# Optimization experiments

Measured on AMD Instinct MI355X. Metric: run time of the kernel, lower is better.

Reference implementation:

```python
import jax, jax.numpy as jnp
import numpy as np

BS, Z, NOBJ = 16384, 512, 64


def setup_inputs() -> dict:
    key = jax.random.key(0)
    ks = jax.random.split(key, 12)
    din = Z + 4  # z concatenated with bounds (x_size = 0)

    def lin(k, i, o):
        kw, kb = jax.random.split(k)
        w = jax.random.normal(kw, (i, o), jnp.float32) * (1.0 / np.sqrt(i))
        b = jax.random.normal(kb, (o,), jnp.float32) * 0.01
        return w, b

    W1, c1 = lin(ks[0], din, 512)
    W2, c2 = lin(ks[1], 512, 256)
    W3, c3 = lin(ks[2], 256, 128)
    W4, c4 = lin(ks[3], 128, 64)
    W5, c5 = lin(ks[4], 64, NOBJ * 4)
    z = jax.random.normal(ks[5], (BS, Z), jnp.float32)
    # room bounds [x_min, y_min, x_max, y_max]; must allow gaps >= 1
    bounds = jnp.array([0.0, 0.0, 40.0, 40.0], jnp.float32)
    return {"z": z, "bounds": bounds,
            "W1": W1, "c1": c1, "W2": W2, "c2": c2, "W3": W3, "c3": c3,
            "W4": W4, "c4": c4, "W5": W5, "c5": c5}


def _lrelu(v):
    return jnp.where(v > 0, v, 0.2 * v)


def _solve_axis(pp, pg, lo, hi):
    """Exact KKT solution of: min (x-pp)^2 + (g-pg)^2  s.t. x>=lo, g>=1, x+g<=hi.
    Returns (x, w) with w = x + g. Matches the parabolic QP per object/axis."""
    x0 = jnp.maximum(pp, lo)          # box projection (lower bounds only)
    g0 = jnp.maximum(pg, 1.0)
    t = 0.5 * (hi - pp - pg)          # projection of (pp,pg) onto line x+g=hi
    xl = jnp.clip(pp + t, lo, hi - 1.0)
    over = (x0 + g0) > hi             # coupling constraint active?
    x = jnp.where(over, xl, x0)
    g = jnp.where(over, hi - xl, g0)
    return x, x + g


def reference(z, bounds, W1, c1, W2, c2, W3, c3, W4, c4, W5, c5):
    bs = z.shape[0]
    bnd = jnp.broadcast_to(bounds, (bs, 4))
    h = jnp.concatenate([z, bnd], axis=1)          # (bs, z_size+4)
    h = _lrelu(h @ W1 + c1)                        # dropout treated as eval/identity
    h = _lrelu(h @ W2 + c2)
    h = _lrelu(h @ W3 + c3)
    h = _lrelu(h @ W4 + c4)
    p = (h @ W5 + c5).reshape(bs, NOBJ, 4)         # per-object params [px, py, pw, ph]
    px, py, pw, ph = p[..., 0], p[..., 1], p[..., 2], p[..., 3]
    b0, b1, b2, b3 = bounds[0], bounds[1], bounds[2], bounds[3]
    # QP objective: sum (x-px)^2+(y-py)^2+((w-x)-pw)^2+((h-y)-ph)^2
    # s.t. x>=b0, y>=b1, w<=b2, h<=b3, x<=w-1, y<=h-1. Separable per object/axis.
    xs, ws = _solve_axis(px, pw, b0, b2)
    ys, hs = _solve_axis(py, ph, b1, b3)
    return jnp.stack([xs, ys, ws, hs], axis=-1)    # (bs, num_objs, 4)
```

## Files before the change

kernel.cpp:

```cpp
#include <hip/hip_runtime.h>


#define MROWS 16384

typedef __attribute__((ext_vector_type(8))) short bf16x8;
typedef __attribute__((ext_vector_type(4))) float floatx4;

__device__ __forceinline__ unsigned short f2bf(float x) {
    union { float f; unsigned u; } c; c.f = x;
    unsigned r = c.u + 0x7fffu + ((c.u >> 16) & 1u);
    return (unsigned short)(r >> 16);
}
__device__ __forceinline__ float bf2f(unsigned short b) {
    union { unsigned u; float f; } c; c.u = ((unsigned)b) << 16;
    return c.f;
}

__device__ __forceinline__ bf16x8 gload(const unsigned short* p) {
    bf16x8 r;
    asm volatile("global_load_dwordx4 %0, %1, off"
                 : "=&v"(r)
                 : "v"((unsigned long long)(size_t)p)
                 : "memory");
    return r;
}
template<int IMM>
__device__ __forceinline__ void vwait(bf16x8& v) {
    asm volatile("s_waitcnt vmcnt(%1)" : "+v"(v) : "n"(IMM) : "memory");
}
__device__ __forceinline__ void drain8(bf16x8 (&r)[8]) {
    asm volatile("s_waitcnt vmcnt(0)"
                 : "+v"(r[0]), "+v"(r[1]), "+v"(r[2]), "+v"(r[3]),
                   "+v"(r[4]), "+v"(r[5]), "+v"(r[6]), "+v"(r[7])
                 :: "memory");
}
__device__ __forceinline__ void drain4(bf16x8 (&r)[4]) {
    asm volatile("s_waitcnt vmcnt(0)"
                 : "+v"(r[0]), "+v"(r[1]), "+v"(r[2]), "+v"(r[3])
                 :: "memory");
}

__global__ __launch_bounds__(256) void pack_wt(
    const float* __restrict__ W1, unsigned short* __restrict__ T1,
    const float* __restrict__ W2, unsigned short* __restrict__ T2,
    const float* __restrict__ W3, unsigned short* __restrict__ T3,
    const float* __restrict__ W4, unsigned short* __restrict__ T4,
    const float* __restrict__ W5, unsigned short* __restrict__ T5)
{
    const int idx = blockIdx.x * 256 + threadIdx.x;
    if (blockIdx.y == 4) {
        if (idx >= 256 * 64) return;
        const int k = idx >> 8, n = idx & 255;
        const float v = W5[idx];
        const unsigned short hi = f2bf(v);
        const unsigned short lo = f2bf(v - bf2f(hi));
        const int ntile = n >> 4, m_l = n & 15;
        const int ks = k >> 5, quad = (k >> 3) & 3, e = k & 7;
        const size_t b = (size_t)(((ks * 16 + ntile) * 2) * 64 + quad * 16 + m_l) * 8 + e;
        T5[b] = hi; T5[b + 512] = lo;
        return;
    }
    const float* W; unsigned short* T; int Kreal, nshift;
    switch (blockIdx.y) {
        case 0:  W = W1; T = T1; Kreal = 516; nshift = 9; break;
        case 1:  W = W2; T = T2; Kreal = 512; nshift = 8; break;
        case 2:  W = W3; T = T3; Kreal = 256; nshift = 7; break;
        default: W = W4; T = T4; Kreal = 128; nshift = 6; break;
    }
    const int N = 1 << nshift, NT = N >> 4;
    const int KS = (Kreal + 31) >> 5;
    if (idx >= N * KS * 32) return;
    const int k = idx >> nshift;
    const int n = idx & (N - 1);
    const unsigned short v = (k < Kreal) ? f2bf(W[idx]) : (unsigned short)0;
    const int ntile = n >> 4, m_l = n & 15;
    const int ks = k >> 5, quad = (k >> 3) & 3, e = k & 7;
    T[(size_t)((ks * NT + ntile) * 64 + quad * 16 + m_l) * 8 + e] = v;
}

#define OFF_ZS   0
#define LD_ZS    552
#define OFF_H1   17664
#define LD_H1    520
#define OFF_H2   0
#define LD_H2    264
#define OFF_H3   17664
#define LD_H3    136
#define OFF_H4   8448
#define LD_H4    72
#define OFF_P    17664
#define LD_P     260
#define LDS_TOT  34304

template<int NF, int KSTEPS, int NT, int DEP>
__device__ __forceinline__ void layer_stream(
    unsigned short* lds, int offA, int lda, int offC, int ldc,
    const unsigned short* __restrict__ Wt,
    const float* __restrict__ bias, int wid, int lane)
{
    const int m_l = lane & 15, quad = lane >> 4;
    constexpr int NFR = NF * KSTEPS;
    const unsigned short* __restrict__ Wb = Wt + ((size_t)(wid * NF) * 64 + lane) * 8;

    floatx4 acc[2][NF];
    #pragma unroll
    for (int j = 0; j < NF; ++j) {
        const float bv = bias[wid * (NF * 16) + j * 16 + m_l];
        acc[0][j] = (floatx4){bv, bv, bv, bv};
        acc[1][j] = (floatx4){bv, bv, bv, bv};
    }

    bf16x8 ring[DEP];
    #pragma unroll
    for (int f = 0; f < DEP; ++f) {
        const int g = (f < NFR) ? f : 0;
        ring[f] = gload(Wb + (size_t)((g / NF) * NT + (g % NF)) * 512);
    }
    bf16x8 a0, a1;
    #pragma unroll
    for (int f = 0; f < NFR; ++f) {
        const int ks = f / NF, j = f - ks * NF;
        if (j == 0) {
            a0 = *(const bf16x8*)&lds[offA + (m_l     ) * lda + ks*32 + quad*8];
            a1 = *(const bf16x8*)&lds[offA + (m_l + 16) * lda + ks*32 + quad*8];
        }
        vwait<DEP - 1>(ring[f % DEP]);
        acc[0][j] = __builtin_amdgcn_mfma_f32_16x16x32_bf16(a0, ring[f % DEP], acc[0][j], 0, 0, 0);
        acc[1][j] = __builtin_amdgcn_mfma_f32_16x16x32_bf16(a1, ring[f % DEP], acc[1][j], 0, 0, 0);
        const int nf2 = (f + DEP < NFR) ? f + DEP : 0;
        ring[f % DEP] = gload(Wb + (size_t)((nf2 / NF) * NT + (nf2 % NF)) * 512);
    }
    if constexpr (DEP == 8) drain8(ring); else drain4(ring);

    #pragma unroll
    for (int j = 0; j < NF; ++j) {
        const int col = wid * (NF * 16) + j * 16 + m_l;
        #pragma unroll
        for (int i = 0; i < 2; ++i)
            #pragma unroll
            for (int r = 0; r < 4; ++r) {
                float v = acc[i][j][r];
                v = v > 0.f ? v : 0.2f * v;
                lds[offC + (i*16 + quad*4 + r) * ldc + col] = f2bf(v);
            }
    }
}

__global__ __launch_bounds__(256, 2) void fused_mlp_qp(
    const float* __restrict__ z, const float* __restrict__ bounds,
    const unsigned short* __restrict__ Wt1, const float* __restrict__ c1,
    const unsigned short* __restrict__ Wt2, const float* __restrict__ c2,
    const unsigned short* __restrict__ Wt3, const float* __restrict__ c3,
    const unsigned short* __restrict__ Wt4, const float* __restrict__ c4,
    const unsigned short* __restrict__ Wt5, const float* __restrict__ c5,
    float* __restrict__ out)
{
    __shared__ unsigned short lds[LDS_TOT];
    const int tid  = threadIdx.x;
    const int wid  = tid >> 6, lane = tid & 63;
    const int m_l  = lane & 15, quad = lane >> 4;
    const int bm   = blockIdx.x * 32;

    const float4 bnd = *(const float4*)bounds;

    {
        const float4* __restrict__ zf = (const float4*)(z + (size_t)bm * 512);
        #pragma unroll
        for (int i = 0; i < 16; ++i) {
            const int f   = i * 256 + tid;
            const int row = f >> 7, c4i = f & 127;
            const float4 v = zf[f];
            unsigned short t4[4] = {f2bf(v.x), f2bf(v.y), f2bf(v.z), f2bf(v.w)};
            *(uint2*)&lds[OFF_ZS + row * LD_ZS + c4i * 4] = *(uint2*)t4;
        }
        if (tid < 160) {
            const int row = tid / 5, j = tid % 5;
            unsigned short t8[8] = {0,0,0,0,0,0,0,0};
            if (j == 0) { t8[0] = f2bf(bnd.x); t8[1] = f2bf(bnd.y);
                          t8[2] = f2bf(bnd.z); t8[3] = f2bf(bnd.w); }
            *(uint4*)&lds[OFF_ZS + row * LD_ZS + 512 + j * 8] = *(uint4*)t8;
        }
    }
    __syncthreads();

    layer_stream<8,17,32,8>(lds, OFF_ZS, LD_ZS, OFF_H1, LD_H1, Wt1, c1, wid, lane);
    __syncthreads();
    layer_stream<4,16,16,8>(lds, OFF_H1, LD_H1, OFF_H2, LD_H2, Wt2, c2, wid, lane);
    __syncthreads();
    layer_stream<2,8, 8, 8>(lds, OFF_H2, LD_H2, OFF_H3, LD_H3, Wt3, c3, wid, lane);
    __syncthreads();
    layer_stream<1,4, 4, 4>(lds, OFF_H3, LD_H3, OFF_H4, LD_H4, Wt4, c4, wid, lane);
    __syncthreads();

    {
        const unsigned short* __restrict__ Wb5 = Wt5 + (size_t)wid * 4096 + (size_t)lane * 8;
        floatx4 acc[2][4];
        #pragma unroll
        for (int j = 0; j < 4; ++j) {
            const float bv = c5[wid * 64 + j * 16 + m_l];
            acc[0][j] = (floatx4){bv, bv, bv, bv};
            acc[1][j] = (floatx4){bv, bv, bv, bv};
        }
        auto w5off = [](int g) {
            const int ks = g >> 3, rem = g & 7;
            return (size_t)ks * 16384 + (size_t)(rem >> 1) * 1024 + (size_t)(rem & 1) * 512;
        };
        bf16x8 ring[8];
        #pragma unroll
        for (int f = 0; f < 8; ++f) ring[f] = gload(Wb5 + w5off(f));
        bf16x8 a0, a1;
        #pragma unroll
        for (int f = 0; f < 16; ++f) {
            const int ks = f >> 3, rem = f & 7, j = rem >> 1;
            if (rem == 0) {
                a0 = *(const bf16x8*)&lds[OFF_H4 + (m_l     ) * LD_H4 + ks*32 + quad*8];
                a1 = *(const bf16x8*)&lds[OFF_H4 + (m_l + 16) * LD_H4 + ks*32 + quad*8];
            }
            vwait<7>(ring[f & 7]);
            acc[0][j] = __builtin_amdgcn_mfma_f32_16x16x32_bf16(a0, ring[f & 7], acc[0][j], 0, 0, 0);
            acc[1][j] = __builtin_amdgcn_mfma_f32_16x16x32_bf16(a1, ring[f & 7], acc[1][j], 0, 0, 0);
            const int nf2 = (f + 8 < 16) ? f + 8 : 0;
            ring[f & 7] = gload(Wb5 + w5off(nf2));
        }
        drain8(ring);

        float* __restrict__ p = (float*)&lds[OFF_P];
        #pragma unroll
        for (int j = 0; j < 4; ++j) {
            const int col = wid * 64 + j * 16 + m_l;
            #pragma unroll
            for (int i = 0; i < 2; ++i)
                #pragma unroll
                for (int r = 0; r < 4; ++r)
                    p[(i*16 + quad*4 + r) * LD_P + col] = acc[i][j][r];
        }
    }
    __syncthreads();

    const float b0 = bnd.x, b1 = bnd.y, b2 = bnd.z, b3 = bnd.w;
    const float* __restrict__ p = (const float*)&lds[OFF_P];
    #pragma unroll
    for (int i = 0; i < 8; ++i) {
        const int row = i * 4 + wid;
        const float4 pv = *(const float4*)&p[row * LD_P + lane * 4];
        float xs, wo, ys, ho;
        {
            const float px = pv.x, pw = pv.z;
            const float x0 = fmaxf(px, b0);
            const float g0 = fmaxf(pw, 1.0f);
            const float t  = 0.5f * (b2 - px - pw);
            const float xl = fminf(fmaxf(px + t, b0), b2 - 1.0f);
            const bool over = (x0 + g0) > b2;
            const float x = over ? xl : x0;
            const float g = over ? (b2 - xl) : g0;
            xs = x; wo = x + g;
        }
        {
            const float py = pv.y, ph = pv.w;
            const float x0 = fmaxf(py, b1);
            const float g0 = fmaxf(ph, 1.0f);
            const float t  = 0.5f * (b3 - py - ph);
            const float xl = fminf(fmaxf(py + t, b1), b3 - 1.0f);
            const bool over = (x0 + g0) > b3;
            const float x = over ? xl : x0;
            const float g = over ? (b3 - xl) : g0;
            ys = x; ho = x + g;
        }
        float4 o; o.x = xs; o.y = ys; o.z = wo; o.w = ho;
        ((float4*)out)[(size_t)(bm + row) * 64 + lane] = o;
    }
}

extern "C" void kernel_launch(void* const* d_in, const int* in_sizes, int n_in,
                              void* d_out, int out_size, void* d_ws, size_t ws_size,
                              hipStream_t stream) {
    const float* z      = (const float*)d_in[0];
    const float* bounds = (const float*)d_in[1];
    const float* W1 = (const float*)d_in[2];
    const float* c1 = (const float*)d_in[3];
    const float* W2 = (const float*)d_in[4];
    const float* c2 = (const float*)d_in[5];
    const float* W3 = (const float*)d_in[6];
    const float* c3 = (const float*)d_in[7];
    const float* W4 = (const float*)d_in[8];
    const float* c4 = (const float*)d_in[9];
    const float* W5 = (const float*)d_in[10];
    const float* c5 = (const float*)d_in[11];
    float* out = (float*)d_out;

    unsigned short* ws  = (unsigned short*)d_ws;
    unsigned short* Wt1 = ws;
    unsigned short* Wt2 = Wt1 + 278528;
    unsigned short* Wt3 = Wt2 + 131072;
    unsigned short* Wt4 = Wt3 + 32768;
    unsigned short* Wt5 = Wt4 + 8192;

    pack_wt<<<dim3(1088, 5), 256, 0, stream>>>(
        W1, Wt1, W2, Wt2, W3, Wt3, W4, Wt4, W5, Wt5);
    fused_mlp_qp<<<dim3(MROWS / 32), 256, 0, stream>>>(
        z, bounds, Wt1, c1, Wt2, c2, Wt3, c3, Wt4, c4, Wt5, c5, out);
}
```

Baseline: 124.7 us.

## Double row tile to 64 per block with 8 waves and vectorize weight packing

The fused MLP block now handles 64 rows with 512 threads (8 waves). Each wave computes 4 M-fragments per streamed weight fragment, which halves per-row weight traffic from L2 and reuses each B fragment across more MFMAs. LDS usage doubles to about 134 KB, which may limit occupancy to one block per CU. The weight-pack kernel now has each thread build 8 K-elements and write them with one 16-byte store, replacing per-element scattered stores.

Result: faster. 120.5 us (-3.4%).

```diff
diff --git a/kernel.cpp b/kernel.cpp
--- a/kernel.cpp
+++ b/kernel.cpp
@@ -49,15 +49,20 @@
 {
     const int idx = blockIdx.x * 256 + threadIdx.x;
     if (blockIdx.y == 4) {
-        if (idx >= 256 * 64) return;
-        const int k = idx >> 8, n = idx & 255;
-        const float v = W5[idx];
-        const unsigned short hi = f2bf(v);
-        const unsigned short lo = f2bf(v - bf2f(hi));
+        if (idx >= 2048) return;
+        const int k8 = idx >> 8, n = idx & 255;
+        const int ks = k8 >> 2, quad = k8 & 3;
         const int ntile = n >> 4, m_l = n & 15;
-        const int ks = k >> 5, quad = (k >> 3) & 3, e = k & 7;
-        const size_t b = (size_t)(((ks * 16 + ntile) * 2) * 64 + quad * 16 + m_l) * 8 + e;
-        T5[b] = hi; T5[b + 512] = lo;
+        unsigned short hi8[8], lo8[8];
+        #pragma unroll
+        for (int e = 0; e < 8; ++e) {
+            const float v = W5[(k8 * 8 + e) * 256 + n];
+            const unsigned short hi = f2bf(v);
+            hi8[e] = hi; lo8[e] = f2bf(v - bf2f(hi));
+        }
+        const size_t b = (size_t)(((ks * 16 + ntile) * 2) * 64 + quad * 16 + m_l) * 8;
+        *(uint4*)&T5[b]       = *(const uint4*)hi8;
+        *(uint4*)&T5[b + 512] = *(const uint4*)lo8;
         return;
     }
     const float* W; unsigned short* T; int Kreal, nshift;
@@ -69,45 +74,50 @@
     }
     const int N = 1 << nshift, NT = N >> 4;
     const int KS = (Kreal + 31) >> 5;
-    if (idx >= N * KS * 32) return;
-    const int k = idx >> nshift;
-    const int n = idx & (N - 1);
-    const unsigned short v = (k < Kreal) ? f2bf(W[idx]) : (unsigned short)0;
+    if (idx >= N * KS * 4) return;
+    const int k8 = idx >> nshift, n = idx & (N - 1);
+    const int ks = k8 >> 2, quad = k8 & 3;
     const int ntile = n >> 4, m_l = n & 15;
-    const int ks = k >> 5, quad = (k >> 3) & 3, e = k & 7;
-    T[(size_t)((ks * NT + ntile) * 64 + quad * 16 + m_l) * 8 + e] = v;
+    unsigned short t8[8];
+    #pragma unroll
+    for (int e = 0; e < 8; ++e) {
+        const int k = k8 * 8 + e;
+        t8[e] = (k < Kreal) ? f2bf(W[(size_t)k * N + n]) : (unsigned short)0;
+    }
+    *(uint4*)&T[(size_t)((ks * NT + ntile) * 64 + quad * 16 + m_l) * 8] = *(const uint4*)t8;
 }
 
 #define OFF_ZS   0
 #define LD_ZS    552
-#define OFF_H1   17664
+#define OFF_H1   35328
 #define LD_H1    520
 #define OFF_H2   0
 #define LD_H2    264
-#define OFF_H3   17664
+#define OFF_H3   16896
 #define LD_H3    136
-#define OFF_H4   8448
+#define OFF_H4   25600
 #define LD_H4    72
-#define OFF_P    17664
+#define OFF_P    35328
 #define LD_P     260
-#define LDS_TOT  34304
-
-template<int NF, int KSTEPS, int NT, int DEP>
+#define LDS_TOT  68608
+
+template<int MR, int NF, int KSTEPS, int NT, int DEP>
 __device__ __forceinline__ void layer_stream(
     unsigned short* lds, int offA, int lda, int offC, int ldc,
     const unsigned short* __restrict__ Wt,
-    const float* __restrict__ bias, int wid, int lane)
+    const float* __restrict__ bias, int ntile0, int rowbase, int lane)
 {
     const int m_l = lane & 15, quad = lane >> 4;
     constexpr int NFR = NF * KSTEPS;
-    const unsigned short* __restrict__ Wb = Wt + ((size_t)(wid * NF) * 64 + lane) * 8;
-
-    floatx4 acc[2][NF];
+    const unsigned short* __restrict__ Wb = Wt + ((size_t)ntile0 * 64 + lane) * 8;
+
+    floatx4 acc[MR][NF];
     #pragma unroll
     for (int j = 0; j < NF; ++j) {
-        const float bv = bias[wid * (NF * 16) + j * 16 + m_l];
-        acc[0][j] = (floatx4){bv, bv, bv, bv};
-        acc[1][j] = (floatx4){bv, bv, bv, bv};
+        const float bv = bias[ntile0 * 16 + j * 16 + m_l];
+        #pragma unroll
+        for (int m = 0; m < MR; ++m)
+            acc[m][j] = (floatx4){bv, bv, bv, bv};
     }
 
     bf16x8 ring[DEP];
@@ -116,17 +126,19 @@
         const int g = (f < NFR) ? f : 0;
         ring[f] = gload(Wb + (size_t)((g / NF) * NT + (g % NF)) * 512);
     }
-    bf16x8 a0, a1;
+    bf16x8 a[MR];
     #pragma unroll
     for (int f = 0; f < NFR; ++f) {
         const int ks = f / NF, j = f - ks * NF;
         if (j == 0) {
-            a0 = *(const bf16x8*)&lds[offA + (m_l     ) * lda + ks*32 + quad*8];
-            a1 = *(const bf16x8*)&lds[offA + (m_l + 16) * lda + ks*32 + quad*8];
+            #pragma unroll
+            for (int m = 0; m < MR; ++m)
+                a[m] = *(const bf16x8*)&lds[offA + (rowbase + m*16 + m_l) * lda + ks*32 + quad*8];
         }
         vwait<DEP - 1>(ring[f % DEP]);
-        acc[0][j] = __builtin_amdgcn_mfma_f32_16x16x32_bf16(a0, ring[f % DEP], acc[0][j], 0, 0, 0);
-        acc[1][j] = __builtin_amdgcn_mfma_f32_16x16x32_bf16(a1, ring[f % DEP], acc[1][j], 0, 0, 0);
+        #pragma unroll
+        for (int m = 0; m < MR; ++m)
+            acc[m][j] = __builtin_amdgcn_mfma_f32_16x16x32_bf16(a[m], ring[f % DEP], acc[m][j], 0, 0, 0);
         const int nf2 = (f + DEP < NFR) ? f + DEP : 0;
         ring[f % DEP] = gload(Wb + (size_t)((nf2 / NF) * NT + (nf2 % NF)) * 512);
     }
@@ -134,19 +146,19 @@
 
     #pragma unroll
     for (int j = 0; j < NF; ++j) {
-        const int col = wid * (NF * 16) + j * 16 + m_l;
-        #pragma unroll
-        for (int i = 0; i < 2; ++i)
+        const int col = ntile0 * 16 + j * 16 + m_l;
+        #pragma unroll
+        for (int m = 0; m < MR; ++m)
             #pragma unroll
             for (int r = 0; r < 4; ++r) {
-                float v = acc[i][j][r];
+                float v = acc[m][j][r];
                 v = v > 0.f ? v : 0.2f * v;
-                lds[offC + (i*16 + quad*4 + r) * ldc + col] = f2bf(v);
+                lds[offC + (rowbase + m*16 + quad*4 + r) * ldc + col] = f2bf(v);
             }
     }
 }
 
-__global__ __launch_bounds__(256, 2) void fused_mlp_qp(
+__global__ __launch_bounds__(512, 2) void fused_mlp_qp(
     const float* __restrict__ z, const float* __restrict__ bounds,
     const unsigned short* __restrict__ Wt1, const float* __restrict__ c1,
     const unsigned short* __restrict__ Wt2, const float* __restrict__ c2,
@@ -159,7 +171,7 @@
     const int tid  = threadIdx.x;
     const int wid  = tid >> 6, lane = tid & 63;
     const int m_l  = lane & 15, quad = lane >> 4;
-    const int bm   = blockIdx.x * 32;
+    const int bm   = blockIdx.x * 64;
 
     const float4 bnd = *(const float4*)bounds;
 
@@ -167,13 +179,13 @@
         const float4* __restrict__ zf = (const float4*)(z + (size_t)bm * 512);
         #pragma unroll
         for (int i = 0; i < 16; ++i) {
-            const int f   = i * 256 + tid;
+            const int f   = i * 512 + tid;
             const int row = f >> 7, c4i = f & 127;
             const float4 v = zf[f];
             unsigned short t4[4] = {f2bf(v.x), f2bf(v.y), f2bf(v.z), f2bf(v.w)};
             *(uint2*)&lds[OFF_ZS + row * LD_ZS + c4i * 4] = *(uint2*)t4;
         }
-        if (tid < 160) {
+        if (tid < 320) {
             const int row = tid / 5, j = tid % 5;
             unsigned short t8[8] = {0,0,0,0,0,0,0,0};
             if (j == 0) { t8[0] = f2bf(bnd.x); t8[1] = f2bf(bnd.y);
@@ -183,56 +195,59 @@
     }
     __syncthreads();
 
-    layer_stream<8,17,32,8>(lds, OFF_ZS, LD_ZS, OFF_H1, LD_H1, Wt1, c1, wid, lane);
-    __syncthreads();
-    layer_stream<4,16,16,8>(lds, OFF_H1, LD_H1, OFF_H2, LD_H2, Wt2, c2, wid, lane);
-    __syncthreads();
-    layer_stream<2,8, 8, 8>(lds, OFF_H2, LD_H2, OFF_H3, LD_H3, Wt3, c3, wid, lane);
-    __syncthreads();
-    layer_stream<1,4, 4, 4>(lds, OFF_H3, LD_H3, OFF_H4, LD_H4, Wt4, c4, wid, lane);
+    layer_stream<4,2,17,32,8>(lds, OFF_ZS, LD_ZS, OFF_H1, LD_H1, Wt1, c1, wid*4,     0, lane);
+    layer_stream<4,2,17,32,8>(lds, OFF_ZS, LD_ZS, OFF_H1, LD_H1, Wt1, c1, wid*4 + 2, 0, lane);
+    __syncthreads();
+    layer_stream<4,2,16,16,8>(lds, OFF_H1, LD_H1, OFF_H2, LD_H2, Wt2, c2, wid*2, 0, lane);
+    __syncthreads();
+    layer_stream<4,1, 8, 8,8>(lds, OFF_H2, LD_H2, OFF_H3, LD_H3, Wt3, c3, wid, 0, lane);
+    __syncthreads();
+    layer_stream<2,1, 4, 4,4>(lds, OFF_H3, LD_H3, OFF_H4, LD_H4, Wt4, c4, wid & 3, (wid >> 2) * 32, lane);
     __syncthreads();
 
     {
-        const unsigned short* __restrict__ Wb5 = Wt5 + (size_t)wid * 4096 + (size_t)lane * 8;
-        floatx4 acc[2][4];
-        #pragma unroll
-        for (int j = 0; j < 4; ++j) {
-            const float bv = c5[wid * 64 + j * 16 + m_l];
-            acc[0][j] = (floatx4){bv, bv, bv, bv};
-            acc[1][j] = (floatx4){bv, bv, bv, bv};
+        const unsigned short* __restrict__ Wb5 = Wt5 + (size_t)wid * 2048 + (size_t)lane * 8;
+        floatx4 acc[4][2];
+        #pragma unroll
+        for (int j = 0; j < 2; ++j) {
+            const float bv = c5[wid * 32 + j * 16 + m_l];
+            #pragma unroll
+            for (int m = 0; m < 4; ++m)
+                acc[m][j] = (floatx4){bv, bv, bv, bv};
         }
         auto w5off = [](int g) {
-            const int ks = g >> 3, rem = g & 7;
+            const int ks = g >> 2, rem = g & 3;
             return (size_t)ks * 16384 + (size_t)(rem >> 1) * 1024 + (size_t)(rem & 1) * 512;
         };
         bf16x8 ring[8];
         #pragma unroll
         for (int f = 0; f < 8; ++f) ring[f] = gload(Wb5 + w5off(f));
-        bf16x8 a0, a1;
-        #pragma unroll
-        for (int f = 0; f < 16; ++f) {
-            const int ks = f >> 3, rem = f & 7, j = rem >> 1;
+        bf16x8 a[4];
+        #pragma unroll
+        for (int f = 0; f < 8; ++f) {
+            const int ks = f >> 2, rem = f & 3, j = rem >> 1;
             if (rem == 0) {
-                a0 = *(const bf16x8*)&lds[OFF_H4 + (m_l     ) * LD_H4 + ks*32 + quad*8];
-                a1 = *(const bf16x8*)&lds[OFF_H4 + (m_l + 16) * LD_H4 + ks*32 + quad*8];
+                #pragma unroll
+                for (int m = 0; m < 4; ++m)
+                    a[m] = *(const bf16x8*)&lds[OFF_H4 + (m*16 + m_l) * LD_H4 + ks*32 + quad*8];
             }
-            vwait<7>(ring[f & 7]);
-            acc[0][j] = __builtin_amdgcn_mfma_f32_16x16x32_bf16(a0, ring[f & 7], acc[0][j], 0, 0, 0);
-            acc[1][j] = __builtin_amdgcn_mfma_f32_16x16x32_bf16(a1, ring[f & 7], acc[1][j], 0, 0, 0);
-            const int nf2 = (f + 8 < 16) ? f + 8 : 0;
-            ring[f & 7] = gload(Wb5 + w5off(nf2));
+            vwait<7>(ring[f]);
+            #pragma unroll
+            for (int m = 0; m < 4; ++m)
+                acc[m][j] = __builtin_amdgcn_mfma_f32_16x16x32_bf16(a[m], ring[f], acc[m][j], 0, 0, 0);
+            ring[f] = gload(Wb5 + w5off(0));
         }
         drain8(ring);
 
         float* __restrict__ p = (float*)&lds[OFF_P];
         #pragma unroll
-        for (int j = 0; j < 4; ++j) {
-            const int col = wid * 64 + j * 16 + m_l;
-            #pragma unroll
-            for (int i = 0; i < 2; ++i)
+        for (int j = 0; j < 2; ++j) {
+            const int col = wid * 32 + j * 16 + m_l;
+            #pragma unroll
+            for (int m = 0; m < 4; ++m)
                 #pragma unroll
                 for (int r = 0; r < 4; ++r)
-                    p[(i*16 + quad*4 + r) * LD_P + col] = acc[i][j][r];
+                    p[(m*16 + quad*4 + r) * LD_P + col] = acc[m][j][r];
         }
     }
     __syncthreads();
@@ -241,7 +256,7 @@
     const float* __restrict__ p = (const float*)&lds[OFF_P];
     #pragma unroll
     for (int i = 0; i < 8; ++i) {
-        const int row = i * 4 + wid;
+        const int row = i * 8 + wid;
         const float4 pv = *(const float4*)&p[row * LD_P + lane * 4];
         float xs, wo, ys, ho;
         {
@@ -295,8 +310,8 @@
     unsigned short* Wt4 = Wt3 + 32768;
     unsigned short* Wt5 = Wt4 + 8192;
 
-    pack_wt<<<dim3(1088, 5), 256, 0, stream>>>(
+    pack_wt<<<dim3(136, 5), 256, 0, stream>>>(
         W1, Wt1, W2, Wt2, W3, Wt3, W4, Wt4, W5, Wt5);
-    fused_mlp_qp<<<dim3(MROWS / 32), 256, 0, stream>>>(
+    fused_mlp_qp<<<dim3(MROWS / 64), 512, 0, stream>>>(
         z, bounds, Wt1, c1, Wt2, c2, Wt3, c3, Wt4, c4, Wt5, c5, out);
 }
```
